# Performance work log

Measured on AMD Instinct MI355X. Metric: run time of the kernel, lower is better.

Reference implementation:

```python
import jax, jax.numpy as jnp
import numpy as np

N, M, C, CSKIP, K = 16384, 4096, 256, 128, 3
BIG = 1e10  # distance penalty for cross-batch pairs


def setup_inputs() -> dict:
    key = jax.random.key(0)
    ks = jax.random.split(key, 6)
    return {
        "x": jax.random.normal(ks[0], (M, C), jnp.float32),
        "pos": jax.random.normal(ks[1], (M, 3), jnp.float32),
        "batch": jnp.zeros((M,), jnp.int32),
        "x_skip": jax.random.normal(ks[2], (N, CSKIP), jnp.float32),
        "pos_skip": jax.random.normal(ks[3], (N, 3), jnp.float32),
        "batch_skip": jnp.zeros((N,), jnp.int32),
        "W1": jax.random.normal(ks[4], (C + CSKIP, 256), jnp.float32) * (1.0 / np.sqrt(C + CSKIP)),
        "b1": jnp.zeros((256,), jnp.float32),
        "W2": jax.random.normal(ks[5], (256, 256), jnp.float32) * (1.0 / np.sqrt(256)),
        "b2": jnp.zeros((256,), jnp.float32),
    }


def _knn_idx(pos, pos_skip, batch, batch_skip, k):
    # Squared distances via GEMM form: [N, M]
    a2 = jnp.sum(pos_skip * pos_skip, axis=-1, keepdims=True)      # [N,1]
    b2 = jnp.sum(pos * pos, axis=-1)[None, :]                       # [1,M]
    d2 = a2 + b2 - 2.0 * (pos_skip @ pos.T)                         # [N,M]
    d2 = jnp.where(batch_skip[:, None] != batch[None, :], BIG, d2)
    _, idx = jax.lax.top_k(-d2, k)                                  # [N,k]
    return idx


def reference(x, pos, batch, x_skip, pos_skip, batch_skip, W1, b1, W2, b2):
    idx = _knn_idx(pos, pos_skip, batch, batch_skip, K)             # [N,k] coarse neighbor ids
    # Exact squared dist recomputed from gathered positions (matches torch diff path)
    diff = pos_skip[:, None, :] - pos[idx]                          # [N,k,3]
    d2 = jnp.sum(diff * diff, axis=-1, keepdims=True)               # [N,k,1]
    w = 1.0 / (d2 + 1e-8)                                           # inverse-distance weights
    wsum = jnp.sum(w, axis=1, keepdims=True)                        # per-row scatter_add == sum over k
    w = w / (wsum + 1e-8)
    x_interp = jnp.sum(w * x[idx], axis=1)                          # [N,C]
    h = jnp.concatenate([x_interp, x_skip], axis=1)                 # [N,C+C']
    h = jax.nn.relu(h @ W1 + b1)
    h = jax.nn.relu(h @ W2 + b2)
    return h
```

## Files before the change

kernel.cpp:

```cpp
#include <hip/hip_runtime.h>

typedef float     f4   __attribute__((ext_vector_type(4)));
typedef float     f32x4 __attribute__((ext_vector_type(4)));
typedef _Float16  h8   __attribute__((ext_vector_type(8)));
typedef _Float16  h4   __attribute__((ext_vector_type(4)));
typedef _Float16  h2   __attribute__((ext_vector_type(2)));

#define NQ   16384
#define MP   4096
#define CF   256
#define CSK  128
#define K1   384
#define HID  256
#define QBK  64

__device__ __forceinline__ unsigned umed3(unsigned a, unsigned b, unsigned c) {
    unsigned r;
    asm("v_med3_u32 %0, %1, %2, %3" : "=v"(r) : "v"(a), "v"(b), "v"(c));
    return r;
}

__global__ __launch_bounds__(256) void wconv_kernel(
    const float* __restrict__ W1, const float* __restrict__ W2,
    _Float16* __restrict__ Wt1, _Float16* __restrict__ Wt2)
{
    const int i = blockIdx.x * 256 + threadIdx.x;
    if (i < K1 * HID) {
        const int k = i >> 8, n = i & 255;
        Wt1[(size_t)(k >> 5) * 8192 + ((k >> 3) & 3) * 2048 + n * 8 + (k & 7)]
            = (_Float16)W1[i];
    } else {
        const int i2 = i - K1 * HID;
        const int k = i2 >> 8, n = i2 & 255;
        Wt2[(size_t)(k >> 5) * 8192 + ((k >> 3) & 3) * 2048 + n * 8 + (k & 7)]
            = (_Float16)W2[i2];
    }
}

__global__ __launch_bounds__(512, 1) void fused_kernel(
    const float* __restrict__ pos,
    const float* __restrict__ pos_skip,
    const float* __restrict__ x,
    const float* __restrict__ x_skip,
    const _Float16* __restrict__ Wt1,
    const _Float16* __restrict__ Wt2,
    const float* __restrict__ b1,
    const float* __restrict__ b2,
    float* __restrict__ out)
{
    __shared__ __align__(16) char smem[51712];
    _Float16* pxh = (_Float16*)smem;
    _Float16* pyh = (_Float16*)(smem + 8192);
    _Float16* pzh = (_Float16*)(smem + 16384);
    unsigned short (*ci)[48] = (unsigned short (*)[48])(smem + 24576);
    _Float16 (*As)[392] = (_Float16 (*)[392])smem;
    _Float16 (*Hs)[264] = (_Float16 (*)[264])smem;
    int   (*fidx)[3] = (int (*)[3])(smem + 50176);
    float (*fw)[3]   = (float (*)[3])(smem + 50944);

    const int tid = threadIdx.x;

    {
        const f4* posv = (const f4*)pos;
        for (int m = tid; m < MP / 4; m += 512) {
            const f4 a = posv[3*m], b = posv[3*m+1], c = posv[3*m+2];
            h4 hx, hy, hz;
            hx[0]=(_Float16)a[0]; hx[1]=(_Float16)a[3];
            hx[2]=(_Float16)b[2]; hx[3]=(_Float16)c[1];
            hy[0]=(_Float16)a[1]; hy[1]=(_Float16)b[0];
            hy[2]=(_Float16)b[3]; hy[3]=(_Float16)c[2];
            hz[0]=(_Float16)a[2]; hz[1]=(_Float16)b[1];
            hz[2]=(_Float16)c[0]; hz[3]=(_Float16)c[3];
            *(h4*)&pxh[4*m] = hx;
            *(h4*)&pyh[4*m] = hy;
            *(h4*)&pzh[4*m] = hz;
        }
    }
    __syncthreads();

    const int lane = tid & 63;
    const int wv   = tid >> 6;

    {
        h2 q2x[8], q2y[8], q2z[8];
        #pragma unroll
        for (int k = 0; k < 8; k++) {
            const int q = blockIdx.x * QBK + wv * 8 + k;
            const _Float16 hx = (_Float16)pos_skip[3*q+0];
            const _Float16 hy = (_Float16)pos_skip[3*q+1];
            const _Float16 hz = (_Float16)pos_skip[3*q+2];
            q2x[k][0] = hx; q2x[k][1] = hx;
            q2y[k][0] = hy; q2y[k][1] = hy;
            q2z[k][0] = hz; q2z[k][1] = hz;
        }

        unsigned K0[8], K1v[8], K2[8];
        #pragma unroll
        for (int k = 0; k < 8; k++) { K0[k] = ~0u; K1v[k] = ~0u; K2[k] = ~0u; }

        #define INS(k, key) {                                              \
            const unsigned o0 = K0[k], o1 = K1v[k], o2 = K2[k];            \
            K0[k]  = min(o0, (key));                                       \
            K1v[k] = umed3(o0, o1, (key));                                 \
            K2[k]  = umed3(o1, o2, (key));                                 \
        }

        union hpack { h4 v4; h2 v2[2]; };
        #define EVALP(CX, CY, CZ, JB)                                      \
            _Pragma("unroll")                                              \
            for (int k = 0; k < 8; k++) {                                  \
                _Pragma("unroll")                                          \
                for (int pp = 0; pp < 2; pp++) {                           \
                    const h2 dx = q2x[k] - (CX).v2[pp];                    \
                    const h2 dy = q2y[k] - (CY).v2[pp];                    \
                    const h2 dz = q2z[k] - (CZ).v2[pp];                    \
                    const h2 dd = dx*dx + dy*dy + dz*dz;                   \
                    const unsigned du = __builtin_bit_cast(unsigned, dd);  \
                    const unsigned key0 = ((du & 0xFFFFu) << 12) + (JB) + pp*2; \
                    const unsigned key1 = ((du >> 16) << 12) + (JB) + pp*2 + 1; \
                    INS(k, key0);                                          \
                    INS(k, key1);                                          \
                }                                                          \
            }

        const h4* px4 = (const h4*)pxh;
        const h4* py4 = (const h4*)pyh;
        const h4* pz4 = (const h4*)pzh;

        hpack cx, cy, cz, nx, ny, nz;
        int idx = lane;
        cx.v4 = px4[idx]; cy.v4 = py4[idx]; cz.v4 = pz4[idx];

        for (int it = 0; it < 16; ++it) {
            const int nidx = idx + 64;
            nx.v4 = px4[nidx]; ny.v4 = py4[nidx]; nz.v4 = pz4[nidx];
            const unsigned jb = (unsigned)(it * 256 + lane * 4);
            EVALP(cx, cy, cz, jb);
            cx = nx; cy = ny; cz = nz;
            idx = nidx;
        }
        #undef EVALP
        #undef INS

        #pragma unroll
        for (int k = 0; k < 8; k++) {
            unsigned a0 = K0[k], a1 = K1v[k], a2 = K2[k];
            {
                const unsigned b0 = (unsigned)__builtin_amdgcn_ds_swizzle((int)a0, 0x041F);
                const unsigned b1 = (unsigned)__builtin_amdgcn_ds_swizzle((int)a1, 0x041F);
                const unsigned b2 = (unsigned)__builtin_amdgcn_ds_swizzle((int)a2, 0x041F);
                const unsigned m0 = min(a0, b0);
                const unsigned c1 = max(a0, b0);
                const unsigned d0 = min(a1, b1), d1 = max(a1, b1);
                const unsigned m1 = min(c1, d0);
                const unsigned m2 = min(min(max(c1, d0), d1), min(a2, b2));
                a0 = m0; a1 = m1; a2 = m2;
            }
            {
                const unsigned b0 = (unsigned)__builtin_amdgcn_ds_swizzle((int)a0, 0x081F);
                const unsigned b1 = (unsigned)__builtin_amdgcn_ds_swizzle((int)a1, 0x081F);
                const unsigned b2 = (unsigned)__builtin_amdgcn_ds_swizzle((int)a2, 0x081F);
                const unsigned m0 = min(a0, b0);
                const unsigned c1 = max(a0, b0);
                const unsigned d0 = min(a1, b1), d1 = max(a1, b1);
                const unsigned m1 = min(c1, d0);
                const unsigned m2 = min(min(max(c1, d0), d1), min(a2, b2));
                a0 = m0; a1 = m1; a2 = m2;
            }
            if (!(lane & 3)) {
                const int q = wv * 8 + k;
                const int pr = lane >> 2;
                ci[q][pr*3+0] = (unsigned short)(a0 & 0xFFFu);
                ci[q][pr*3+1] = (unsigned short)(a1 & 0xFFFu);
                ci[q][pr*3+2] = (unsigned short)(a2 & 0xFFFu);
            }
        }
    }
    __syncthreads();

    {
        const int q    = tid >> 3;
        const int part = tid & 7;
        const int g    = blockIdx.x * QBK + q;

        int jarr[6];
        #pragma unroll
        for (int c = 0; c < 6; c++) jarr[c] = ci[q][part*6 + c];
        float pxf[6], pyf[6], pzf[6];
        #pragma unroll
        for (int c = 0; c < 6; c++) {
            pxf[c] = pos[3*jarr[c]+0];
            pyf[c] = pos[3*jarr[c]+1];
            pzf[c] = pos[3*jarr[c]+2];
        }

        const double qxd = (double)pos_skip[3*g+0];
        const double qyd = (double)pos_skip[3*g+1];
        const double qzd = (double)pos_skip[3*g+2];
        const double a2d = qxd*qxd + qyd*qyd + qzd*qzd;

        double e0 = 1e300, e1 = 1e300, e2 = 1e300;
        int    j0 = 0,     j1 = 0,     j2 = 0;
        #pragma unroll
        for (int c = 0; c < 6; c++) {
            const int j = jarr[c];
            const double pxd = (double)pxf[c];
            const double pyd = (double)pyf[c];
            const double pzd = (double)pzf[c];
            const double b2  = pxd*pxd + pyd*pyd + pzd*pzd;
            const double dot = qxd*pxd + qyd*pyd + qzd*pzd;
            const double d   = (a2d + b2) - 2.0 * dot;
            if (d < e2) {
                if (d < e1) {
                    e2 = e1; j2 = j1;
                    if (d < e0) { e1 = e0; j1 = j0; e0 = d; j0 = j; }
                    else        { e1 = d;  j1 = j; }
                } else { e2 = d; j2 = j; }
            }
        }
        ci[q][part*3+0] = (unsigned short)j0;
        ci[q][part*3+1] = (unsigned short)j1;
        ci[q][part*3+2] = (unsigned short)j2;
    }
    __syncthreads();

    if (tid < QBK) {
        const int g = blockIdx.x * QBK + tid;

        int jarr[24];
        #pragma unroll
        for (int c = 0; c < 24; c++) jarr[c] = ci[tid][c];
        float pxf[24], pyf[24], pzf[24];
        #pragma unroll
        for (int c = 0; c < 24; c++) {
            pxf[c] = pos[3*jarr[c]+0];
            pyf[c] = pos[3*jarr[c]+1];
            pzf[c] = pos[3*jarr[c]+2];
        }

        const double qxd = (double)pos_skip[3*g+0];
        const double qyd = (double)pos_skip[3*g+1];
        const double qzd = (double)pos_skip[3*g+2];
        const double a2d = qxd*qxd + qyd*qyd + qzd*qzd;

        double e0 = 1e300, e1 = 1e300, e2 = 1e300;
        int    j0 = 0,     j1 = 0,     j2 = 0;
        #pragma unroll
        for (int c = 0; c < 24; c++) {
            const int j = jarr[c];
            const double pxd = (double)pxf[c];
            const double pyd = (double)pyf[c];
            const double pzd = (double)pzf[c];
            const double b2  = pxd*pxd + pyd*pyd + pzd*pzd;
            const double dot = qxd*pxd + qyd*pyd + qzd*pzd;
            const double d   = (a2d + b2) - 2.0 * dot;
            if (d < e2) {
                if (d < e1) {
                    e2 = e1; j2 = j1;
                    if (d < e0) { e1 = e0; j1 = j0; e0 = d; j0 = j; }
                    else        { e1 = d;  j1 = j; }
                } else { e2 = d; j2 = j; }
            }
        }
        const float sx = pos_skip[3*g+0], sy = pos_skip[3*g+1], sz = pos_skip[3*g+2];
        const int jj[3] = { j0, j1, j2 };
        float wv3[3];
        #pragma unroll
        for (int k = 0; k < 3; k++) {
            const float dx = sx - pos[3*jj[k]+0];
            const float dy = sy - pos[3*jj[k]+1];
            const float dz = sz - pos[3*jj[k]+2];
            const float dd = dx*dx + dy*dy + dz*dz;
            wv3[k] = 1.0f / (dd + 1e-8f);
        }
        const float inv = 1.0f / (wv3[0] + wv3[1] + wv3[2] + 1e-8f);
        #pragma unroll
        for (int k = 0; k < 3; k++) {
            fidx[tid][k] = jj[k];
            fw[tid][k]   = wv3[k] * inv;
        }
    }
    __syncthreads();

    const int row0 = blockIdx.x * QBK;

    {
        const int r   = tid >> 3;
        const int sub = tid & 7;
        const int g   = row0 + r;
        const int j0 = fidx[r][0], j1 = fidx[r][1], j2 = fidx[r][2];
        const float w0 = fw[r][0], w1 = fw[r][1], w2 = fw[r][2];
        const f4* xa = (const f4*)(x + (size_t)j0 * CF);
        const f4* xb = (const f4*)(x + (size_t)j1 * CF);
        const f4* xc = (const f4*)(x + (size_t)j2 * CF);
        const f4* xs = (const f4*)(x_skip + (size_t)g * CSK);
        #pragma unroll
        for (int t = 0; t < 8; t++) {
            const int c4 = t * 8 + sub;
            const f4 a = xa[c4], b = xb[c4], c = xc[c4];
            const f4 v = a * w0 + b * w1 + c * w2;
            h4 hv; hv[0]=(_Float16)v[0]; hv[1]=(_Float16)v[1];
                   hv[2]=(_Float16)v[2]; hv[3]=(_Float16)v[3];
            *(h4*)&As[r][c4 * 4] = hv;
        }
        #pragma unroll
        for (int t = 0; t < 4; t++) {
            const int c4 = t * 8 + sub;
            const f4 v = xs[c4];
            h4 hv; hv[0]=(_Float16)v[0]; hv[1]=(_Float16)v[1];
                   hv[2]=(_Float16)v[2]; hv[3]=(_Float16)v[3];
            *(h4*)&As[r][CF + c4 * 4] = hv;
        }
    }

    const int ln   = tid & 15;
    const int quad = (tid >> 4) & 3;
    const int nb   = wv * 32;
    const int q8   = quad * 8;

    const _Float16* w1b = Wt1 + quad * 2048 + (size_t)(nb + ln) * 8;
    const _Float16* w2b = Wt2 + quad * 2048 + (size_t)(nb + ln) * 8;

    f32x4 acc[4][2];
    #pragma unroll
    for (int rg = 0; rg < 4; rg++)
        #pragma unroll
        for (int nt = 0; nt < 2; nt++) acc[rg][nt] = (f32x4)0.0f;

    h8 B[4][2];
    #pragma unroll
    for (int s = 0; s < 4; s++)
        #pragma unroll
        for (int nt = 0; nt < 2; nt++)
            B[s][nt] = *(const h8*)(w1b + (size_t)s * 8192 + nt * 128);

    __syncthreads();

    #pragma unroll
    for (int kb = 0; kb < 12; kb++) {
        const int s = kb & 3;
        h8 hb[2];
        #pragma unroll
        for (int nt = 0; nt < 2; nt++) hb[nt] = B[s][nt];
        const int nk = kb + 4;
        if (nk < 12) {
            #pragma unroll
            for (int nt = 0; nt < 2; nt++)
                B[s][nt] = *(const h8*)(w1b + (size_t)nk * 8192 + nt * 128);
        } else {
            #pragma unroll
            for (int nt = 0; nt < 2; nt++)
                B[s][nt] = *(const h8*)(w2b + (size_t)(nk - 12) * 8192 + nt * 128);
        }
        #pragma unroll
        for (int rg = 0; rg < 4; rg++) {
            const h8 ha = *(const h8*)&As[rg * 16 + ln][kb * 32 + q8];
            #pragma unroll
            for (int nt = 0; nt < 2; nt++)
                acc[rg][nt] = __builtin_amdgcn_mfma_f32_16x16x32_f16(ha, hb[nt], acc[rg][nt], 0, 0, 0);
        }
    }
    __syncthreads();

    #pragma unroll
    for (int nt = 0; nt < 2; nt++) {
        const int n = nb + nt * 16 + ln;
        const float bv = b1[n];
        #pragma unroll
        for (int rg = 0; rg < 4; rg++) {
            #pragma unroll
            for (int r = 0; r < 4; r++) {
                Hs[rg * 16 + quad * 4 + r][n] =
                    (_Float16)fmaxf(acc[rg][nt][r] + bv, 0.0f);
            }
            acc[rg][nt] = (f32x4)0.0f;
        }
    }
    __syncthreads();

    #pragma unroll
    for (int kb = 0; kb < 8; kb++) {
        const int s = kb & 3;
        h8 hb[2];
        #pragma unroll
        for (int nt = 0; nt < 2; nt++) hb[nt] = B[s][nt];
        const int nk = kb + 4;
        if (nk < 8) {
            #pragma unroll
            for (int nt = 0; nt < 2; nt++)
                B[s][nt] = *(const h8*)(w2b + (size_t)nk * 8192 + nt * 128);
        }
        #pragma unroll
        for (int rg = 0; rg < 4; rg++) {
            const h8 ha = *(const h8*)&Hs[rg * 16 + ln][kb * 32 + q8];
            #pragma unroll
            for (int nt = 0; nt < 2; nt++)
                acc[rg][nt] = __builtin_amdgcn_mfma_f32_16x16x32_f16(ha, hb[nt], acc[rg][nt], 0, 0, 0);
        }
    }

    #pragma unroll
    for (int nt = 0; nt < 2; nt++) {
        const int n = nb + nt * 16 + ln;
        const float bv = b2[n];
        #pragma unroll
        for (int rg = 0; rg < 4; rg++) {
            #pragma unroll
            for (int r = 0; r < 4; r++) {
                const int m = rg * 16 + quad * 4 + r;
                out[(size_t)(row0 + m) * HID + n] = fmaxf(acc[rg][nt][r] + bv, 0.0f);
            }
        }
    }
}

extern "C" void kernel_launch(void* const* d_in, const int* in_sizes, int n_in,
                              void* d_out, int out_size, void* d_ws, size_t ws_size,
                              hipStream_t stream) {
    const float* x         = (const float*)d_in[0];
    const float* pos       = (const float*)d_in[1];
    const float* x_skip    = (const float*)d_in[3];
    const float* pos_skip  = (const float*)d_in[4];
    const float* W1        = (const float*)d_in[6];
    const float* b1        = (const float*)d_in[7];
    const float* W2        = (const float*)d_in[8];
    const float* b2        = (const float*)d_in[9];
    float* out = (float*)d_out;

    char* ws = (char*)d_ws;
    _Float16* Wt1 = (_Float16*)ws;
    _Float16* Wt2 = (_Float16*)(ws + 196608);

    wconv_kernel<<<(K1*HID + HID*HID) / 256, 256, 0, stream>>>(W1, W2, Wt1, Wt2);
    fused_kernel<<<NQ / QBK, 512, 0, stream>>>(pos, pos_skip, x, x_skip,
                                               Wt1, Wt2, b1, b2, out);
}
```

Before: 120.8 us.

## Split fused kernel into two-half KNN kernel and separate MLP kernel

The single fused kernel is split in two. A KNN kernel runs twice as many blocks, each scanning half of the candidate points and writing its top-3 indices to workspace. An MLP kernel then merges the two partial top-3 lists with exact double-precision distances and runs the interpolation and GEMMs. The aim is more parallelism and occupancy, with launch bounds raised to 2 blocks and the KNN shared memory reduced. The cost is an extra launch and a global round trip for the indices.

```diff
diff --git a/kernel.cpp b/kernel.cpp
--- a/kernel.cpp
+++ b/kernel.cpp
@@ -37,44 +37,35 @@
     }
 }
 
-__global__ __launch_bounds__(512, 1) void fused_kernel(
+__global__ __launch_bounds__(512, 2) void knn_kernel(
     const float* __restrict__ pos,
     const float* __restrict__ pos_skip,
-    const float* __restrict__ x,
-    const float* __restrict__ x_skip,
-    const _Float16* __restrict__ Wt1,
-    const _Float16* __restrict__ Wt2,
-    const float* __restrict__ b1,
-    const float* __restrict__ b2,
-    float* __restrict__ out)
+    unsigned short* __restrict__ fidx6_g)
 {
-    __shared__ __align__(16) char smem[51712];
+    __shared__ __align__(16) char smem[18432];
     _Float16* pxh = (_Float16*)smem;
-    _Float16* pyh = (_Float16*)(smem + 8192);
-    _Float16* pzh = (_Float16*)(smem + 16384);
-    unsigned short (*ci)[48] = (unsigned short (*)[48])(smem + 24576);
-    _Float16 (*As)[392] = (_Float16 (*)[392])smem;
-    _Float16 (*Hs)[264] = (_Float16 (*)[264])smem;
-    int   (*fidx)[3] = (int (*)[3])(smem + 50176);
-    float (*fw)[3]   = (float (*)[3])(smem + 50944);
-
-    const int tid = threadIdx.x;
+    _Float16* pyh = (_Float16*)(smem + 4096);
+    _Float16* pzh = (_Float16*)(smem + 8192);
+    unsigned short (*ci)[48] = (unsigned short (*)[48])(smem + 12288);
+
+    const int tid  = threadIdx.x;
+    const int half = blockIdx.x & 1;
+    const int qblk = blockIdx.x >> 1;
 
     {
         const f4* posv = (const f4*)pos;
-        for (int m = tid; m < MP / 4; m += 512) {
-            const f4 a = posv[3*m], b = posv[3*m+1], c = posv[3*m+2];
-            h4 hx, hy, hz;
-            hx[0]=(_Float16)a[0]; hx[1]=(_Float16)a[3];
-            hx[2]=(_Float16)b[2]; hx[3]=(_Float16)c[1];
-            hy[0]=(_Float16)a[1]; hy[1]=(_Float16)b[0];
-            hy[2]=(_Float16)b[3]; hy[3]=(_Float16)c[2];
-            hz[0]=(_Float16)a[2]; hz[1]=(_Float16)b[1];
-            hz[2]=(_Float16)c[0]; hz[3]=(_Float16)c[3];
-            *(h4*)&pxh[4*m] = hx;
-            *(h4*)&pyh[4*m] = hy;
-            *(h4*)&pzh[4*m] = hz;
-        }
+        const int m = half * 512 + tid;
+        const f4 a = posv[3*m], b = posv[3*m+1], c = posv[3*m+2];
+        h4 hx, hy, hz;
+        hx[0]=(_Float16)a[0]; hx[1]=(_Float16)a[3];
+        hx[2]=(_Float16)b[2]; hx[3]=(_Float16)c[1];
+        hy[0]=(_Float16)a[1]; hy[1]=(_Float16)b[0];
+        hy[2]=(_Float16)b[3]; hy[3]=(_Float16)c[2];
+        hz[0]=(_Float16)a[2]; hz[1]=(_Float16)b[1];
+        hz[2]=(_Float16)c[0]; hz[3]=(_Float16)c[3];
+        *(h4*)&pxh[4*tid] = hx;
+        *(h4*)&pyh[4*tid] = hy;
+        *(h4*)&pzh[4*tid] = hz;
     }
     __syncthreads();
 
@@ -85,7 +76,7 @@
         h2 q2x[8], q2y[8], q2z[8];
         #pragma unroll
         for (int k = 0; k < 8; k++) {
-            const int q = blockIdx.x * QBK + wv * 8 + k;
+            const int q = qblk * QBK + wv * 8 + k;
             const _Float16 hx = (_Float16)pos_skip[3*q+0];
             const _Float16 hy = (_Float16)pos_skip[3*q+1];
             const _Float16 hz = (_Float16)pos_skip[3*q+2];
@@ -131,10 +122,11 @@
         int idx = lane;
         cx.v4 = px4[idx]; cy.v4 = py4[idx]; cz.v4 = pz4[idx];
 
-        for (int it = 0; it < 16; ++it) {
+        const unsigned jbase = (unsigned)(half * 2048);
+        for (int it = 0; it < 8; ++it) {
             const int nidx = idx + 64;
             nx.v4 = px4[nidx]; ny.v4 = py4[nidx]; nz.v4 = pz4[nidx];
-            const unsigned jb = (unsigned)(it * 256 + lane * 4);
+            const unsigned jb = jbase + (unsigned)(it * 256 + lane * 4);
             EVALP(cx, cy, cz, jb);
             cx = nx; cy = ny; cz = nz;
             idx = nidx;
@@ -181,7 +173,7 @@
     {
         const int q    = tid >> 3;
         const int part = tid & 7;
-        const int g    = blockIdx.x * QBK + q;
+        const int g    = qblk * QBK + q;
 
         int jarr[6];
         #pragma unroll
@@ -225,7 +217,7 @@
     __syncthreads();
 
     if (tid < QBK) {
-        const int g = blockIdx.x * QBK + tid;
+        const int g = qblk * QBK + tid;
 
         int jarr[24];
         #pragma unroll
@@ -262,6 +254,71 @@
                 } else { e2 = d; j2 = j; }
             }
         }
+        fidx6_g[(size_t)g*6 + half*3 + 0] = (unsigned short)j0;
+        fidx6_g[(size_t)g*6 + half*3 + 1] = (unsigned short)j1;
+        fidx6_g[(size_t)g*6 + half*3 + 2] = (unsigned short)j2;
+    }
+}
+
+__global__ __launch_bounds__(512, 2) void mlp_kernel(
+    const float* __restrict__ pos,
+    const float* __restrict__ pos_skip,
+    const float* __restrict__ x,
+    const float* __restrict__ x_skip,
+    const _Float16* __restrict__ Wt1,
+    const _Float16* __restrict__ Wt2,
+    const float* __restrict__ b1,
+    const float* __restrict__ b2,
+    const unsigned short* __restrict__ fidx6_g,
+    float* __restrict__ out)
+{
+    __shared__ __align__(16) char smem[51712];
+    _Float16 (*As)[392] = (_Float16 (*)[392])smem;
+    _Float16 (*Hs)[264] = (_Float16 (*)[264])smem;
+    int   (*fidx)[3] = (int (*)[3])(smem + 50176);
+    float (*fw)[3]   = (float (*)[3])(smem + 50944);
+
+    const int tid  = threadIdx.x;
+    const int row0 = blockIdx.x * QBK;
+
+    if (tid < QBK) {
+        const int g = row0 + tid;
+
+        int jarr[6];
+        #pragma unroll
+        for (int c = 0; c < 6; c++) jarr[c] = fidx6_g[(size_t)g*6 + c];
+        float pxf[6], pyf[6], pzf[6];
+        #pragma unroll
+        for (int c = 0; c < 6; c++) {
+            pxf[c] = pos[3*jarr[c]+0];
+            pyf[c] = pos[3*jarr[c]+1];
+            pzf[c] = pos[3*jarr[c]+2];
+        }
+
+        const double qxd = (double)pos_skip[3*g+0];
+        const double qyd = (double)pos_skip[3*g+1];
+        const double qzd = (double)pos_skip[3*g+2];
+        const double a2d = qxd*qxd + qyd*qyd + qzd*qzd;
+
+        double e0 = 1e300, e1 = 1e300, e2 = 1e300;
+        int    j0 = 0,     j1 = 0,     j2 = 0;
+        #pragma unroll
+        for (int c = 0; c < 6; c++) {
+            const int j = jarr[c];
+            const double pxd = (double)pxf[c];
+            const double pyd = (double)pyf[c];
+            const double pzd = (double)pzf[c];
+            const double b2  = pxd*pxd + pyd*pyd + pzd*pzd;
+            const double dot = qxd*pxd + qyd*pyd + qzd*pzd;
+            const double d   = (a2d + b2) - 2.0 * dot;
+            if (d < e2) {
+                if (d < e1) {
+                    e2 = e1; j2 = j1;
+                    if (d < e0) { e1 = e0; j1 = j0; e0 = d; j0 = j; }
+                    else        { e1 = d;  j1 = j; }
+                } else { e2 = d; j2 = j; }
+            }
+        }
         const float sx = pos_skip[3*g+0], sy = pos_skip[3*g+1], sz = pos_skip[3*g+2];
         const int jj[3] = { j0, j1, j2 };
         float wv3[3];
@@ -281,8 +338,6 @@
         }
     }
     __syncthreads();
-
-    const int row0 = blockIdx.x * QBK;
 
     {
         const int r   = tid >> 3;
@@ -315,6 +370,7 @@
 
     const int ln   = tid & 15;
     const int quad = (tid >> 4) & 3;
+    const int wv   = tid >> 6;
     const int nb   = wv * 32;
     const int q8   = quad * 8;
 
@@ -428,10 +484,12 @@
     float* out = (float*)d_out;
 
     char* ws = (char*)d_ws;
-    _Float16* Wt1 = (_Float16*)ws;
-    _Float16* Wt2 = (_Float16*)(ws + 196608);
+    _Float16*       Wt1     = (_Float16*)ws;
+    _Float16*       Wt2     = (_Float16*)(ws + 196608);
+    unsigned short* fidx6_g = (unsigned short*)(ws + 327680);
 
     wconv_kernel<<<(K1*HID + HID*HID) / 256, 256, 0, stream>>>(W1, W2, Wt1, Wt2);
-    fused_kernel<<<NQ / QBK, 512, 0, stream>>>(pos, pos_skip, x, x_skip,
-                                               Wt1, Wt2, b1, b2, out);
+    knn_kernel<<<2 * (NQ / QBK), 512, 0, stream>>>(pos, pos_skip, fidx6_g);
+    mlp_kernel<<<NQ / QBK, 512, 0, stream>>>(pos, pos_skip, x, x_skip,
+                                             Wt1, Wt2, b1, b2, fidx6_g, out);
 }
```

Measured after the change: 124.8 us. 3.3% more time.
